# Optimization experiments

Measured on AMD Instinct MI355X. Metric: run time of the kernel, lower is better.

## Reference

```python
import jax, jax.numpy as jnp
import numpy as np

EPS = 1e-5


def conv3x3(x, w, b):
    # x [B,C,H,W], w [O,C,3,3], stride 1, pad 1
    y = jax.lax.conv_general_dilated(x, w, (1, 1), ((1, 1), (1, 1)),
                                     dimension_numbers=('NCHW', 'OIHW', 'NCHW'))
    return y + b[None, :, None, None]


def bilinear_gather(x, py, px):
    # x [B,C,H,W]; sampling locations py,px [B,K,H,W] -> [B,C,K,H,W]
    # Zero padding outside the image (matches deform_conv CUDA semantics:
    # out-of-bound corner values contribute 0).
    B, C, H, W = x.shape
    K = py.shape[1]
    x_flat = x.reshape(B, C, H * W)
    y0 = jnp.floor(py)
    x0 = jnp.floor(px)
    out = jnp.zeros((B, C, K, H, W), x.dtype)
    for dy in (0.0, 1.0):
        for dx in (0.0, 1.0):
            yi = y0 + dy
            xi = x0 + dx
            wgt = (1.0 - jnp.abs(py - yi)) * (1.0 - jnp.abs(px - xi))  # [B,K,H,W]
            valid = (yi >= 0) & (yi <= H - 1) & (xi >= 0) & (xi <= W - 1)
            idx = (jnp.clip(yi, 0, H - 1).astype(jnp.int32) * W
                   + jnp.clip(xi, 0, W - 1).astype(jnp.int32)).reshape(B, -1)
            vals = jax.vmap(lambda xf, i: xf[:, i])(x_flat, idx)  # [B,C,K*H*W]
            out = out + (wgt * valid)[:, None] * vals.reshape(B, C, K, H, W)
    return out


def setup_inputs() -> dict:
    key = jax.random.key(0)
    k1, k2, k3 = jax.random.split(key, 3)
    B, C, O, H, W = 4, 64, 64, 128, 128
    x = jax.random.normal(k1, (B, C, H, W), jnp.float32)
    # offset predictor: small init so predicted offsets are modest (realistic)
    off_w = 0.01 * jax.random.normal(k2, (18, C, 3, 3), jnp.float32)
    off_b = jnp.zeros((18,), jnp.float32)
    dc_w = jax.random.normal(k3, (O, C, 3, 3), jnp.float32) / np.sqrt(C * 9)
    dc_b = jnp.zeros((O,), jnp.float32)
    gamma = jnp.ones((O,), jnp.float32)
    beta = jnp.zeros((O,), jnp.float32)
    return {"x": x, "off_w": off_w, "off_b": off_b, "dc_w": dc_w,
            "dc_b": dc_b, "gamma": gamma, "beta": beta}


def reference(x, off_w, off_b, dc_w, dc_b, gamma, beta):
    B, C, H, W = x.shape
    O = dc_w.shape[0]
    K = 9  # 3x3 kernel
    offset = conv3x3(x, off_w, off_b)              # [B,18,H,W]
    off = offset.reshape(B, K, 2, H, W)            # (dy,dx) per kernel tap, row-major
    dyo, dxo = off[:, :, 0], off[:, :, 1]          # [B,K,H,W]
    k = (jnp.arange(3) - 1).astype(x.dtype)        # kernel taps {-1,0,1}
    kgy = jnp.repeat(k, 3)                         # [9] row-major y offsets
    kgx = jnp.tile(k, 3)                           # [9] row-major x offsets
    hh = jnp.arange(H, dtype=x.dtype)
    ww = jnp.arange(W, dtype=x.dtype)
    # stride 1, pad 1: base point = out_pos - 1 + tap; pad is folded into kgy/kgx
    py = hh[None, None, :, None] + kgy[None, :, None, None] + dyo
    px = ww[None, None, None, :] + kgx[None, :, None, None] + dxo
    sampled = bilinear_gather(x, py, px)           # [B,C,K,H,W]
    y = jnp.einsum('ock,bckhw->bohw', dc_w.reshape(O, C, K), sampled)
    y = y + dc_b[None, :, None, None]
    # BatchNorm2d (training mode: biased batch statistics)
    mu = y.mean(axis=(0, 2, 3), keepdims=True)
    var = y.var(axis=(0, 2, 3), keepdims=True)
    yn = (y - mu) * jax.lax.rsqrt(var + EPS)
    return jax.nn.relu(yn * gamma[None, :, None, None] + beta[None, :, None, None])
```

## Files before the change

kernel.cpp:

```cpp
#include <hip/hip_runtime.h>

#define HH 128
#define WW 128
#define HWSZ (HH * WW)
#define CC 64
#define OO 64
#define BB 4
#define NOFF 18
#define KK 576

#define WS_BG     0
#define WS_BGO    18432
#define WS_SUMS   27648
#define WS_SUMSQ  27712
#define WS_YBUF   27776

typedef __attribute__((ext_vector_type(8))) short short8;
typedef __attribute__((ext_vector_type(4))) int int4v;
typedef __attribute__((ext_vector_type(4))) float f32x4;

__device__ inline unsigned bf16rne(float f) {
  unsigned u = __float_as_uint(f);
  u += 0x7fff + ((u >> 16) & 1);
  return u >> 16;
}

__global__ __launch_bounds__(256) void prep_kernel(
    const float* __restrict__ x, const float* __restrict__ off_w,
    const float* __restrict__ dc_w, unsigned int* __restrict__ xTu,
    int* __restrict__ Bg, int* __restrict__ Bgo, float* __restrict__ sums) {
  int bid = blockIdx.x;
  if (bid < BB * HH) {
    __shared__ float T[CC][WW + 1];
    int b = bid >> 7, h = bid & 127;
    int tw = threadIdx.x & 127, th = threadIdx.x >> 7;
    const float* xp = x + (size_t)b * CC * HWSZ + h * WW;
#pragma unroll 8
    for (int i = 0; i < 32; ++i) {
      int c = i * 2 + th;
      T[c][tw] = xp[c * HWSZ + tw];
    }
    __syncthreads();
    int c2 = threadIdx.x & 31, wq = threadIdx.x >> 5;
    unsigned int* op = xTu + ((size_t)(b * HH + h) * WW) * 32;
#pragma unroll 8
    for (int i = 0; i < 16; ++i) {
      int w = i * 8 + wq;
      unsigned pk = bf16rne(T[2 * c2][w]) | (bf16rne(T[2 * c2 + 1][w]) << 16);
      op[w * 32 + c2] = pk;
    }
  } else {
    int pb = bid - BB * HH;
    int tid = pb * 256 + threadIdx.x;
    int stride = 64 * 256;
    for (int i = tid; i < 72 * 64 * 4; i += stride) {
      int j = i & 3, o = (i >> 2) & 63, g = i >> 8;
      int k2 = g * 4 + j, t = k2 >> 5, jj = k2 & 31;
      unsigned lo = bf16rne(dc_w[o * KK + (2 * jj) * 9 + t]);
      unsigned hi = bf16rne(dc_w[o * KK + (2 * jj + 1) * 9 + t]);
      Bg[i] = (int)(lo | (hi << 16));
    }
    for (int i = tid; i < 72 * 32 * 4; i += stride) {
      int j = i & 3, o = (i >> 2) & 31, g = i >> 7;
      int k2 = g * 4 + j, t = k2 >> 5, jj = k2 & 31;
      unsigned pk = 0;
      if (o < NOFF) {
        unsigned lo = bf16rne(off_w[o * KK + (2 * jj) * 9 + t]);
        unsigned hi = bf16rne(off_w[o * KK + (2 * jj + 1) * 9 + t]);
        pk = lo | (hi << 16);
      }
      Bgo[i] = (int)pk;
    }
    if (tid < 128) sums[tid] = 0.0f;
  }
}

__global__ __launch_bounds__(256) void fused_kernel(
    const unsigned int* __restrict__ xTu, const int* __restrict__ Bg,
    const int* __restrict__ Bgo, const float* __restrict__ off_b,
    const float* __restrict__ dc_b, float* __restrict__ ybuf,
    float* __restrict__ sums, float* __restrict__ sumsq) {
  __shared__ __align__(16) int A[4 * 16 * 100];
  __shared__ __align__(16) int M[4 * 144 * 4];
  __shared__ float offL[4][NOFF][16];

  int cg = threadIdx.x >> 6, lane = threadIdx.x & 63;
  int b = blockIdx.x >> 8, rem = blockIdx.x & 255;
  int h = rem >> 1, w0 = (rem & 1) * 64;
  int hw0 = h * WW + w0;
  int p0 = cg * 16;
  int n16 = lane & 15, q = lane >> 4;
  int pg = lane >> 3, part = lane & 7;
  const unsigned int* xbu = xTu + (size_t)b * HWSZ * 32;

  f32x4 acc2[2] = {f32x4{0, 0, 0, 0}, f32x4{0, 0, 0, 0}};
#pragma unroll 1
  for (int chunk = 0; chunk < 3; ++chunk) {
    int cy = h + chunk - 1;
    bool vy = (cy >= 0) && (cy < HH);
    int cys = min(max(cy, 0), HH - 1);
#pragma unroll
    for (int tl = 0; tl < 3; ++tl) {
#pragma unroll
      for (int i = 0; i < 2; ++i) {
        int px = i * 8 + pg;
        int cx = w0 + p0 + px + tl - 1;
        bool v = vy && (cx >= 0) && (cx < WW);
        int cxs = min(max(cx, 0), WW - 1);
        int4v val = *(const int4v*)&xbu[(cys * WW + cxs) * 32 + part * 4];
        if (!v) { val.x = 0; val.y = 0; val.z = 0; val.w = 0; }
        *(int4v*)&A[(p0 + px) * 100 + tl * 32 + part * 4] = val;
      }
    }
#pragma unroll 1
    for (int kk = 0; kk < 6; ++kk) {
      int4v av = *(const int4v*)&A[(p0 + n16) * 100 + kk * 16 + q * 4];
      short8 af = __builtin_bit_cast(short8, av);
      int g = chunk * 24 + kk * 4 + q;
#pragma unroll
      for (int nt = 0; nt < 2; ++nt) {
        int4v bv = *(const int4v*)&Bgo[(g * 32 + nt * 16 + n16) * 4];
        short8 bfr = __builtin_bit_cast(short8, bv);
        acc2[nt] = __builtin_amdgcn_mfma_f32_16x16x32_bf16(af, bfr, acc2[nt], 0, 0, 0);
      }
    }
  }
#pragma unroll
  for (int nt = 0; nt < 2; ++nt) {
    int o = nt * 16 + n16;
    if (o < NOFF) {
      float bv = off_b[o];
#pragma unroll
      for (int r = 0; r < 4; ++r) offL[cg][o][q * 4 + r] = acc2[nt][r] + bv;
    }
  }

  int* Mw = M + cg * 144 * 4;
#pragma unroll
  for (int it = 0; it < 3; ++it) {
    int m = it * 64 + lane;
    if (m < 144) {
      int pxl = (unsigned)m / 9u;
      int t = m - pxl * 9;
      float dy = offL[cg][2 * t][pxl];
      float dx = offL[cg][2 * t + 1][pxl];
      float py = (float)(h + t / 3 - 1) + dy;
      float pxf = (float)(w0 + p0 + pxl + (t % 3) - 1) + dx;
      float fy0 = floorf(py), fx0 = floorf(pxf);
      float ay = py - fy0, ax = pxf - fx0;
      int iy0 = (int)fy0, ix0 = (int)fx0;
      int iy1 = iy0 + 1, ix1 = ix0 + 1;
      float wy0 = 1.0f - ay, wy1 = ay, wx0 = 1.0f - ax, wx1 = ax;
      if (!(iy0 >= 0 && iy0 < HH)) wy0 = 0.0f;
      if (!(iy1 >= 0 && iy1 < HH)) wy1 = 0.0f;
      if (!(ix0 >= 0 && ix0 < WW)) wx0 = 0.0f;
      if (!(ix1 >= 0 && ix1 < WW)) wx1 = 0.0f;
      int cy0 = min(max(iy0, 0), HH - 1), cy1 = min(max(iy1, 0), HH - 1);
      int cx0 = min(max(ix0, 0), WW - 1), cx1 = min(max(ix1, 0), WW - 1);
      int4v mv;
      mv.x = (cy0 * WW + cx0) | ((cy0 * WW + cx1) << 16);
      mv.y = (cy1 * WW + cx0) | ((cy1 * WW + cx1) << 16);
      mv.z = (int)(bf16rne(wy0 * wx0) | (bf16rne(wy0 * wx1) << 16));
      mv.w = (int)(bf16rne(wy1 * wx0) | (bf16rne(wy1 * wx1) << 16));
      *(int4v*)&Mw[m * 4] = mv;
    }
  }

  int p = lane >> 5;
  int c2 = lane & 31;
  f32x4 acc[4] = {f32x4{0,0,0,0}, f32x4{0,0,0,0}, f32x4{0,0,0,0}, f32x4{0,0,0,0}};
#pragma unroll 1
  for (int chunk = 0; chunk < 3; ++chunk) {
#pragma unroll 1
    for (int tl = 0; tl < 3; ++tl) {
#pragma unroll 4
      for (int pp = 0; pp < 16; pp += 2) {
        int pxl = pp + p;
        int4v mv = *(const int4v*)&Mw[(pxl * 9 + chunk * 3 + tl) * 4];
        unsigned o00 = mv.x & 0xffff, o01 = ((unsigned)mv.x) >> 16;
        unsigned o10 = mv.y & 0xffff, o11 = ((unsigned)mv.y) >> 16;
        unsigned d00 = xbu[o00 * 32 + c2];
        unsigned d01 = xbu[o01 * 32 + c2];
        unsigned d10 = xbu[o10 * 32 + c2];
        unsigned d11 = xbu[o11 * 32 + c2];
        float w00 = __uint_as_float(((unsigned)mv.z) << 16);
        float w01 = __uint_as_float(((unsigned)mv.z) & 0xffff0000u);
        float w10 = __uint_as_float(((unsigned)mv.w) << 16);
        float w11 = __uint_as_float(((unsigned)mv.w) & 0xffff0000u);
        float slo = w00 * __uint_as_float(d00 << 16);
        slo = fmaf(w01, __uint_as_float(d01 << 16), slo);
        slo = fmaf(w10, __uint_as_float(d10 << 16), slo);
        slo = fmaf(w11, __uint_as_float(d11 << 16), slo);
        float shi = w00 * __uint_as_float(d00 & 0xffff0000u);
        shi = fmaf(w01, __uint_as_float(d01 & 0xffff0000u), shi);
        shi = fmaf(w10, __uint_as_float(d10 & 0xffff0000u), shi);
        shi = fmaf(w11, __uint_as_float(d11 & 0xffff0000u), shi);
        unsigned pk = __builtin_amdgcn_perm(
            __float_as_uint(shi) + 0x8000u,
            __float_as_uint(slo) + 0x8000u, 0x07060302u);
        A[(p0 + pxl) * 100 + tl * 32 + c2] = (int)pk;
      }
    }
#pragma unroll 1
    for (int kk = 0; kk < 6; ++kk) {
      int4v av = *(const int4v*)&A[(p0 + n16) * 100 + kk * 16 + q * 4];
      short8 af = __builtin_bit_cast(short8, av);
      int g = chunk * 24 + kk * 4 + q;
#pragma unroll
      for (int nt = 0; nt < 4; ++nt) {
        int4v bv = *(const int4v*)&Bg[(g * 64 + nt * 16 + n16) * 4];
        short8 bfr = __builtin_bit_cast(short8, bv);
        acc[nt] = __builtin_amdgcn_mfma_f32_16x16x32_bf16(af, bfr, acc[nt], 0, 0, 0);
      }
    }
  }

  float* SW = (float*)&A[cg * 1600];
#pragma unroll
  for (int nt = 0; nt < 4; ++nt) {
    int o = nt * 16 + n16;
    float bv = dc_b[o];
    f32x4 r;
    float s = 0.0f, ss = 0.0f;
#pragma unroll
    for (int r0 = 0; r0 < 4; ++r0) {
      r[r0] = acc[nt][r0] + bv;
      s += r[r0];
      ss += r[r0] * r[r0];
    }
    *(f32x4*)(ybuf + (size_t)(b * OO + o) * HWSZ + hw0 + p0 + q * 4) = r;
    s += __shfl_xor(s, 16);  s += __shfl_xor(s, 32);
    ss += __shfl_xor(ss, 16); ss += __shfl_xor(ss, 32);
    if (lane < 16) {
      SW[nt * 16 + lane] = s;
      SW[64 + nt * 16 + lane] = ss;
    }
  }
  __syncthreads();
  if (threadIdx.x < 64) {
    float ts = 0.0f, tq = 0.0f;
#pragma unroll
    for (int wv = 0; wv < 4; ++wv) {
      const float* Sv = (const float*)&A[wv * 1600];
      ts += Sv[threadIdx.x];
      tq += Sv[64 + threadIdx.x];
    }
    atomicAdd(&sums[threadIdx.x], ts);
    atomicAdd(&sumsq[threadIdx.x], tq);
  }
}

__global__ __launch_bounds__(256) void norm_kernel(
    const float* __restrict__ ybuf, const float* __restrict__ sums,
    const float* __restrict__ sumsq, const float* __restrict__ gamma,
    const float* __restrict__ beta, float* __restrict__ out) {
  int gid = blockIdx.x * 256 + threadIdx.x;
  int flat = gid << 2;
  int o = (flat >> 14) & 63;
  const float invN = 1.0f / (float)(BB * HWSZ);
  float mean = sums[o] * invN;
  float var = sumsq[o] * invN - mean * mean;
  float rstd = rsqrtf(var + 1e-5f);
  float g = gamma[o] * rstd;
  float bta = beta[o] - mean * g;
  float4 v = ((const float4*)ybuf)[gid];
  float4 r;
  r.x = fmaxf(v.x * g + bta, 0.0f);
  r.y = fmaxf(v.y * g + bta, 0.0f);
  r.z = fmaxf(v.z * g + bta, 0.0f);
  r.w = fmaxf(v.w * g + bta, 0.0f);
  ((float4*)out)[gid] = r;
}

extern "C" void kernel_launch(void* const* d_in, const int* in_sizes, int n_in,
                              void* d_out, int out_size, void* d_ws, size_t ws_size,
                              hipStream_t stream) {
  const float* x     = (const float*)d_in[0];
  const float* off_w = (const float*)d_in[1];
  const float* off_b = (const float*)d_in[2];
  const float* dc_w  = (const float*)d_in[3];
  const float* dc_b  = (const float*)d_in[4];
  const float* gamma = (const float*)d_in[5];
  const float* beta  = (const float*)d_in[6];
  float* ws = (float*)d_ws;
  int*   Bg     = (int*)(ws + WS_BG);
  int*   Bgo    = (int*)(ws + WS_BGO);
  float* sums   = ws + WS_SUMS;
  float* sumsq  = ws + WS_SUMSQ;
  float* ybuf   = ws + WS_YBUF;
  float* out = (float*)d_out;
  unsigned int* xTu = (unsigned int*)d_out;

  prep_kernel<<<BB * HH + 64, 256, 0, stream>>>(x, off_w, dc_w, xTu, Bg, Bgo, sums);
  fused_kernel<<<BB * HWSZ / 64, 256, 0, stream>>>(xTu, Bg, Bgo, off_b, dc_b, ybuf, sums, sumsq);
  norm_kernel<<<BB * OO * HWSZ / (4 * 256), 256, 0, stream>>>(ybuf, sums, sumsq, gamma, beta, out);
}
```

Baseline: 142.8 us.

## Vectorize bilinear gather to 16-byte loads and software-pipeline issue/blend stages

Each lane now gathers four packed channel words per corner with 128-bit loads instead of one 32-bit word. The gather is split into explicit issue and blend macros that are interleaved, so loads for later taps are in flight while earlier taps are blended and stored to LDS. The change also adds a min-blocks hint of 4 to launch_bounds and partially unrolls the MFMA k-loops. The aim is to raise memory-level parallelism and cut instruction count in the latency-bound gather, at the cost of higher register pressure under a tighter occupancy bound, which could cause spills.

```diff
diff --git a/kernel.cpp b/kernel.cpp
--- a/kernel.cpp
+++ b/kernel.cpp
@@ -75,7 +75,44 @@
   }
 }
 
-__global__ __launch_bounds__(256) void fused_kernel(
+#define G_ISSUE(i, TAP, TL, PH)                                               \
+  int4v m##i, da##i, db##i, dc##i, dd##i;                                     \
+  {                                                                           \
+    int pxl_ = (PH) * 8 + p8;                                                 \
+    m##i = *(const int4v*)&Mw[(pxl_ * 9 + (TAP)) * 4];                        \
+    unsigned x_ = (unsigned)m##i.x, y_ = (unsigned)m##i.y;                    \
+    da##i = *(const int4v*)&xbu[(x_ & 0xffffu) * 32 + cq4];                   \
+    db##i = *(const int4v*)&xbu[(x_ >> 16) * 32 + cq4];                       \
+    dc##i = *(const int4v*)&xbu[(y_ & 0xffffu) * 32 + cq4];                   \
+    dd##i = *(const int4v*)&xbu[(y_ >> 16) * 32 + cq4];                       \
+  }
+
+#define G_BLEND(i, TL, PH)                                                    \
+  {                                                                           \
+    int pxl_ = (PH) * 8 + p8;                                                 \
+    float w00_ = __uint_as_float(((unsigned)m##i.z) << 16);                   \
+    float w01_ = __uint_as_float(((unsigned)m##i.z) & 0xffff0000u);           \
+    float w10_ = __uint_as_float(((unsigned)m##i.w) << 16);                   \
+    float w11_ = __uint_as_float(((unsigned)m##i.w) & 0xffff0000u);           \
+    int4v pk_;                                                                \
+    _Pragma("unroll")                                                         \
+    for (int j = 0; j < 4; ++j) {                                             \
+      float slo_ = w00_ * __uint_as_float(((unsigned)da##i[j]) << 16);        \
+      slo_ = fmaf(w01_, __uint_as_float(((unsigned)db##i[j]) << 16), slo_);   \
+      slo_ = fmaf(w10_, __uint_as_float(((unsigned)dc##i[j]) << 16), slo_);   \
+      slo_ = fmaf(w11_, __uint_as_float(((unsigned)dd##i[j]) << 16), slo_);   \
+      float shi_ = w00_ * __uint_as_float(((unsigned)da##i[j]) & 0xffff0000u);\
+      shi_ = fmaf(w01_, __uint_as_float(((unsigned)db##i[j]) & 0xffff0000u), shi_);\
+      shi_ = fmaf(w10_, __uint_as_float(((unsigned)dc##i[j]) & 0xffff0000u), shi_);\
+      shi_ = fmaf(w11_, __uint_as_float(((unsigned)dd##i[j]) & 0xffff0000u), shi_);\
+      pk_[j] = (int)__builtin_amdgcn_perm(__float_as_uint(shi_) + 0x8000u,    \
+                                          __float_as_uint(slo_) + 0x8000u,    \
+                                          0x07060302u);                       \
+    }                                                                         \
+    *(int4v*)&A[(p0 + pxl_) * 100 + (TL) * 32 + cq4] = pk_;                   \
+  }
+
+__global__ __launch_bounds__(256, 4) void fused_kernel(
     const unsigned int* __restrict__ xTu, const int* __restrict__ Bg,
     const int* __restrict__ Bgo, const float* __restrict__ off_b,
     const float* __restrict__ dc_b, float* __restrict__ ybuf,
@@ -112,7 +149,7 @@
         *(int4v*)&A[(p0 + px) * 100 + tl * 32 + part * 4] = val;
       }
     }
-#pragma unroll 1
+#pragma unroll 2
     for (int kk = 0; kk < 6; ++kk) {
       int4v av = *(const int4v*)&A[(p0 + n16) * 100 + kk * 16 + q * 4];
       short8 af = __builtin_bit_cast(short8, av);
@@ -166,42 +203,25 @@
     }
   }
 
-  int p = lane >> 5;
-  int c2 = lane & 31;
+  int p8 = lane >> 3;
+  int cq4 = (lane & 7) * 4;
   f32x4 acc[4] = {f32x4{0,0,0,0}, f32x4{0,0,0,0}, f32x4{0,0,0,0}, f32x4{0,0,0,0}};
 #pragma unroll 1
   for (int chunk = 0; chunk < 3; ++chunk) {
-#pragma unroll 1
-    for (int tl = 0; tl < 3; ++tl) {
-#pragma unroll 4
-      for (int pp = 0; pp < 16; pp += 2) {
-        int pxl = pp + p;
-        int4v mv = *(const int4v*)&Mw[(pxl * 9 + chunk * 3 + tl) * 4];
-        unsigned o00 = mv.x & 0xffff, o01 = ((unsigned)mv.x) >> 16;
-        unsigned o10 = mv.y & 0xffff, o11 = ((unsigned)mv.y) >> 16;
-        unsigned d00 = xbu[o00 * 32 + c2];
-        unsigned d01 = xbu[o01 * 32 + c2];
-        unsigned d10 = xbu[o10 * 32 + c2];
-        unsigned d11 = xbu[o11 * 32 + c2];
-        float w00 = __uint_as_float(((unsigned)mv.z) << 16);
-        float w01 = __uint_as_float(((unsigned)mv.z) & 0xffff0000u);
-        float w10 = __uint_as_float(((unsigned)mv.w) << 16);
-        float w11 = __uint_as_float(((unsigned)mv.w) & 0xffff0000u);
-        float slo = w00 * __uint_as_float(d00 << 16);
-        slo = fmaf(w01, __uint_as_float(d01 << 16), slo);
-        slo = fmaf(w10, __uint_as_float(d10 << 16), slo);
-        slo = fmaf(w11, __uint_as_float(d11 << 16), slo);
-        float shi = w00 * __uint_as_float(d00 & 0xffff0000u);
-        shi = fmaf(w01, __uint_as_float(d01 & 0xffff0000u), shi);
-        shi = fmaf(w10, __uint_as_float(d10 & 0xffff0000u), shi);
-        shi = fmaf(w11, __uint_as_float(d11 & 0xffff0000u), shi);
-        unsigned pk = __builtin_amdgcn_perm(
-            __float_as_uint(shi) + 0x8000u,
-            __float_as_uint(slo) + 0x8000u, 0x07060302u);
-        A[(p0 + pxl) * 100 + tl * 32 + c2] = (int)pk;
-      }
-    }
-#pragma unroll 1
+    int tap0 = chunk * 3;
+    G_ISSUE(0, tap0 + 0, 0, 0)
+    G_ISSUE(1, tap0 + 0, 0, 1)
+    G_ISSUE(2, tap0 + 1, 1, 0)
+    G_BLEND(0, 0, 0)
+    G_ISSUE(3, tap0 + 1, 1, 1)
+    G_BLEND(1, 0, 1)
+    G_ISSUE(4, tap0 + 2, 2, 0)
+    G_BLEND(2, 1, 0)
+    G_ISSUE(5, tap0 + 2, 2, 1)
+    G_BLEND(3, 1, 1)
+    G_BLEND(4, 2, 0)
+    G_BLEND(5, 2, 1)
+#pragma unroll 2
     for (int kk = 0; kk < 6; ++kk) {
       int4v av = *(const int4v*)&A[(p0 + n16) * 100 + kk * 16 + q * 4];
       short8 af = __builtin_bit_cast(short8, av);
```

Measured after the change: 142.6 us. No clear change (-0.2%).
